# Performance work log

Measured on AMD Instinct MI355X. Metric: run time of the kernel, lower is better.

The kernel has to match this reference:

```python
import jax, jax.numpy as jnp
import numpy as np

EOS = 1e-10
N_NODES = 100000
N_EDGES = 1600000
IN_DIM = 256
HID = 64
ALPHA = 0.1
TEMP = 1.0
BIAS = 1e-4


def setup_inputs() -> dict:
    key = jax.random.key(0)
    k1, k2, k3, k4, k5 = jax.random.split(key, 5)
    features = jax.random.normal(k1, (N_NODES, IN_DIM), dtype=jnp.float32)
    edges = jax.random.randint(k2, (2, N_EDGES), 0, N_NODES, dtype=jnp.int64)
    noise = jax.random.uniform(k3, (N_EDGES,), dtype=jnp.float32)
    # params: embedding Linear(input_dim, hidden) and edge_mlp Linear(2*hidden, 1)
    W_emb = jax.random.normal(k4, (IN_DIM, HID), dtype=jnp.float32) / np.sqrt(IN_DIM)
    b_emb = jnp.zeros((HID,), dtype=jnp.float32)
    W_edge = jax.random.normal(k5, (2 * HID,), dtype=jnp.float32) / np.sqrt(2 * HID)
    b_edge = jnp.zeros((), dtype=jnp.float32)
    return {"features": features, "edges": edges, "noise": noise,
            "W_emb": W_emb, "b_emb": b_emb, "W_edge": W_edge, "b_edge": b_edge}


def _edge_weight_norm_both(src, dst, w, n_nodes):
    # DGL EdgeWeightNorm(norm='both'): w_e / sqrt(outdeg_w(src) * indeg_w(dst))
    deg_out = jax.ops.segment_sum(w, src, num_segments=n_nodes)
    deg_in = jax.ops.segment_sum(w, dst, num_segments=n_nodes)
    return w / jnp.sqrt(deg_out[src] * deg_in[dst])


def reference(features, edges, noise, W_emb, b_emb, W_edge, b_edge):
    src, dst = edges[0], edges[1]
    E = src.shape[0]
    # node embedding: relu(Linear(features))
    h = jax.nn.relu(features @ W_emb + b_emb)  # [N, H]
    # edge score: edge_mlp(cat(h[u], h[v])) symmetrized.
    # split W_edge -> score = h[u]@W1 + h[v]@W2 + b  (avoids materializing concat)
    p1 = h @ W_edge[:HID]   # [N]
    p2 = h @ W_edge[HID:]   # [N]
    s1 = p1[src] + p2[dst] + b_edge
    s2 = p1[dst] + p2[src] + b_edge
    raw = (s1 + s2) * 0.5   # [E]
    # gumbel sigmoid sampling
    eps = (BIAS - (1.0 - BIAS)) * noise + (1.0 - BIAS)
    gate = jnp.log(eps) - jnp.log1p(-eps)
    weights_lp = jax.nn.sigmoid((gate + raw) / TEMP)  # [E]
    weights_hp = 1.0 - weights_lp
    # weight_to_adj: add self loops with weight 1, then EdgeWeightNorm 'both'
    loop = jnp.arange(N_NODES, dtype=src.dtype)
    src_f = jnp.concatenate([src, loop])
    dst_f = jnp.concatenate([dst, loop])
    ones_n = jnp.ones((N_NODES,), dtype=weights_lp.dtype)
    w_lp_full = jnp.concatenate([weights_lp, ones_n]) + EOS
    w_lp_norm = _edge_weight_norm_both(src_f, dst_f, w_lp_full, N_NODES)
    w_hp_full = jnp.concatenate([weights_hp, ones_n]) + EOS
    w_hp_norm = _edge_weight_norm_both(src_f, dst_f, w_hp_full, N_NODES)
    w_hp_norm = w_hp_norm * (-ALPHA)
    w_hp_norm = w_hp_norm.at[E:].set(1.0)  # self-loop weights forced to 1
    return (w_lp_norm, w_hp_norm, weights_lp, weights_hp)
```

## Files before the change

kernel.cpp:

```cpp
#include <hip/hip_runtime.h>
#include <hip/hip_bf16.h>
#include <math.h>

#define N_NODESC 100000
#define N_EDGESC 1600000
#define IN_DIMC 256
#define HIDC 64
#define ALPHAC 0.1f
#define BIASC 1e-4f
#define EOSC 1e-10f

#define MC (N_EDGESC + N_NODESC)
#define NBUCK 25
#define BCAP 68000u
#define W20SCALE 1048576.0f
#define W20INV (1.0f / 1048576.0f)
#define SUMMASK ((1ull << 40) - 1)
#define CNTONE (1ull << 40)

typedef __attribute__((ext_vector_type(8))) short short8;
typedef __attribute__((ext_vector_type(4))) float f32x4;

#define WT_STRIDE 264

__device__ inline void load_edge(const int* __restrict__ edges, int e, int is64,
                                 int& src, int& dst) {
    if (is64) {
        const int2 a = ((const int2*)edges)[e];
        const int2 b = ((const int2*)edges)[N_EDGESC + e];
        src = a.x; dst = b.x;
    } else {
        src = edges[e];
        dst = edges[N_EDGESC + e];
    }
}

__device__ inline short pkbf(float x) {
    union { __hip_bfloat16 b; short s; } u;
    u.b = __float2bfloat16(x);
    return u.s;
}

__global__ __launch_bounds__(256, 4) void node_kernel(
    const float* __restrict__ features,
    const float* __restrict__ W_emb,
    const float* __restrict__ b_emb,
    const float* __restrict__ W_edge,
    const int* __restrict__ edges,
    float* __restrict__ q,
    int* __restrict__ flag) {
    __shared__ __align__(16) short Wt[HIDC * WT_STRIDE];
    const int tid = threadIdx.x;
    if (blockIdx.x == 0 && tid == 0) {
        int z = 0;
        #pragma unroll
        for (int i = 0; i < 16; ++i) z |= edges[2 * i + 1];
        *flag = (z == 0) ? 1 : 0;
    }
    {
        const float4* Wg = (const float4*)W_emb;
        #pragma unroll
        for (int i = 0; i < 16; ++i) {
            const int f4 = tid + 256 * i;
            const float4 g = Wg[f4];
            const int flat = 4 * f4;
            const int k = flat >> 6;
            const int j0 = flat & 63;
            Wt[(j0 + 0) * WT_STRIDE + k] = pkbf(g.x);
            Wt[(j0 + 1) * WT_STRIDE + k] = pkbf(g.y);
            Wt[(j0 + 2) * WT_STRIDE + k] = pkbf(g.z);
            Wt[(j0 + 3) * WT_STRIDE + k] = pkbf(g.w);
        }
    }
    const int lane = tid & 63;
    const int wave = tid >> 6;
    const int quad = lane >> 4;
    const int m = lane & 15;
    f32x4 acc[4];
    float wsum4[4];
    #pragma unroll
    for (int nt = 0; nt < 4; ++nt) {
        const int j = m + 16 * nt;
        const float b = b_emb[j];
        acc[nt] = (f32x4){b, b, b, b};
        wsum4[nt] = W_edge[j] + W_edge[HIDC + j];
    }
    __syncthreads();

    const int node0 = blockIdx.x * 64 + wave * 16;
    const int row = min(node0 + m, N_NODESC - 1);
    const float* frow = features + (size_t)row * IN_DIMC;

    #pragma unroll
    for (int ks = 0; ks < 8; ++ks) {
        const int kk = ks * 32 + quad * 8;
        const float4 fa = *(const float4*)(frow + kk);
        const float4 fb = *(const float4*)(frow + kk + 4);
        short8 af;
        af[0] = pkbf(fa.x); af[1] = pkbf(fa.y);
        af[2] = pkbf(fa.z); af[3] = pkbf(fa.w);
        af[4] = pkbf(fb.x); af[5] = pkbf(fb.y);
        af[6] = pkbf(fb.z); af[7] = pkbf(fb.w);
        #pragma unroll
        for (int nt = 0; nt < 4; ++nt) {
            const short8 bf =
                *(const short8*)&Wt[(m + 16 * nt) * WT_STRIDE + kk];
            acc[nt] = __builtin_amdgcn_mfma_f32_16x16x32_bf16(af, bf, acc[nt],
                                                              0, 0, 0);
        }
    }

    #pragma unroll
    for (int r = 0; r < 4; ++r) {
        float s = 0.f;
        #pragma unroll
        for (int nt = 0; nt < 4; ++nt)
            s = fmaf(fmaxf(acc[nt][r], 0.f), wsum4[nt], s);
        s += __shfl_xor(s, 1);
        s += __shfl_xor(s, 2);
        s += __shfl_xor(s, 4);
        s += __shfl_xor(s, 8);
        if (m == 0) {
            const int node = node0 + quad * 4 + r;
            if (node < N_NODESC) q[node] = s;
        }
    }
}

__global__ __launch_bounds__(256) void edge_scatter(
    const int* __restrict__ edges,
    const float* __restrict__ noise,
    const float* __restrict__ b_edge,
    const float* __restrict__ q,
    unsigned* __restrict__ cursorS,
    unsigned* __restrict__ cursorD,
    float* __restrict__ out,
    const int* __restrict__ flag) {
    __shared__ unsigned histS[NBUCK], histD[NBUCK];
    __shared__ unsigned baseS[NBUCK], baseD[NBUCK];
    const int tid = threadIdx.x;
    if (tid < NBUCK) { histS[tid] = 0; histD[tid] = 0; }
    __syncthreads();
    const int is64 = *flag;
    const float be = b_edge[0];
    int srcA[4], dstA[4];
    float wlpA[4];
    unsigned rkS[4], rkD[4];
    const int e0 = blockIdx.x * 1024 + tid;
    #pragma unroll
    for (int i = 0; i < 4; ++i) {
        const int e = e0 + i * 256;
        srcA[i] = -1;
        if (e < N_EDGESC) {
            int s, d;
            load_edge(edges, e, is64, s, d);
            srcA[i] = s; dstA[i] = d;
            const float raw = 0.5f * (q[s] + q[d]) + be;
            const float u = noise[e];
            const float eps = (BIASC - (1.0f - BIASC)) * u + (1.0f - BIASC);
            const float gate = logf(eps) - log1pf(-eps);
            const float wlp = 1.0f / (1.0f + expf(-(gate + raw)));
            wlpA[i] = wlp;
            out[2 * MC + e] = wlp;
            out[2 * MC + N_EDGESC + e] = 1.0f - wlp;
            rkS[i] = atomicAdd(&histS[s >> 12], 1u);
            rkD[i] = atomicAdd(&histD[d >> 12], 1u);
        }
    }
    __syncthreads();
    if (tid < NBUCK)
        baseS[tid] = atomicAdd(&cursorS[tid], histS[tid]);
    else if (tid < 2 * NBUCK)
        baseD[tid - NBUCK] = atomicAdd(&cursorD[tid - NBUCK], histD[tid - NBUCK]);
    __syncthreads();
    unsigned* recS = (unsigned*)out;
    unsigned* recD = (unsigned*)out + MC;
    #pragma unroll
    for (int i = 0; i < 4; ++i) {
        if (srcA[i] >= 0) {
            const int s = srcA[i], d = dstA[i];
            const unsigned w20 =
                min((unsigned)(wlpA[i] * W20SCALE + 0.5f), 0xFFFFFu);
            const unsigned pS = baseS[s >> 12] + rkS[i];
            const unsigned pD = baseD[d >> 12] + rkD[i];
            if (pS < BCAP)
                recS[(unsigned)(s >> 12) * BCAP + pS] =
                    ((unsigned)(s & 4095) << 20) | w20;
            if (pD < BCAP)
                recD[(unsigned)(d >> 12) * BCAP + pD] =
                    ((unsigned)(d & 4095) << 20) | w20;
        }
    }
}

__global__ __launch_bounds__(1024) void gather_kernel(
    const float* __restrict__ out,
    const unsigned* __restrict__ cursorS,
    const unsigned* __restrict__ cursorD,
    unsigned long long* __restrict__ accS,
    unsigned long long* __restrict__ accD) {
    __shared__ unsigned long long table[4096];
    const int bid = blockIdx.x;
    const int isD = bid >= NBUCK;
    const int bkt = isD ? bid - NBUCK : bid;
    const unsigned* rec = (const unsigned*)out + (isD ? MC : 0) +
                          (unsigned)bkt * BCAP;
    const unsigned cnt = min((isD ? cursorD : cursorS)[bkt], BCAP);
    const int tid = threadIdx.x;
    #pragma unroll
    for (int i = 0; i < 4; ++i) table[tid + 1024 * i] = 0ull;
    __syncthreads();
    for (unsigned i = tid; i < cnt; i += 1024) {
        const unsigned r = rec[i];
        atomicAdd(&table[r >> 20], CNTONE | (unsigned long long)(r & 0xFFFFFu));
    }
    __syncthreads();
    unsigned long long* acc = isD ? accD : accS;
    const int node0 = bkt << 12;
    #pragma unroll
    for (int i = 0; i < 4; ++i) {
        const int local = tid + 1024 * i;
        const int node = node0 + local;
        if (node < N_NODESC) acc[node] = table[local];
    }
}

__global__ __launch_bounds__(256) void prep_kernel(
    const unsigned long long* __restrict__ accS,
    const unsigned long long* __restrict__ accD,
    float4* __restrict__ rnode) {
    const int n = blockIdx.x * blockDim.x + threadIdx.x;
    if (n >= N_NODESC) return;
    const unsigned long long a = accS[n];
    const unsigned long long b = accD[n];
    const float sumS = (float)(a & SUMMASK) * W20INV;
    const float cntS = (float)(a >> 40);
    const float sumD = (float)(b & SUMMASK) * W20INV;
    const float cntD = (float)(b >> 40);
    float4 r;
    r.x = rsqrtf(1.0f + sumS);
    r.y = rsqrtf(1.0f + sumD);
    r.z = rsqrtf(1.0f + cntS - sumS);
    r.w = rsqrtf(1.0f + cntD - sumD);
    rnode[n] = r;
}

__global__ __launch_bounds__(256) void final_kernel(
    const int* __restrict__ edges,
    const float4* __restrict__ rnode,
    float* __restrict__ out,
    const int* __restrict__ flag) {
    const int i = blockIdx.x * blockDim.x + threadIdx.x;
    if (i >= MC) return;
    if (i < N_EDGESC) {
        const int is64 = *flag;
        int src, dst;
        load_edge(edges, i, is64, src, dst);
        const float wlp = out[2 * MC + i] + EOSC;
        const float whp = out[2 * MC + N_EDGESC + i] + EOSC;
        const float4 rs = rnode[src];
        const float4 rd = rnode[dst];
        out[i] = wlp * rs.x * rd.y;
        out[MC + i] = -ALPHAC * whp * rs.z * rd.w;
    } else {
        const int n = i - N_EDGESC;
        const float4 r = rnode[n];
        out[i] = (1.0f + EOSC) * r.x * r.y;
        out[MC + i] = 1.0f;
    }
}

extern "C" void kernel_launch(void* const* d_in, const int* in_sizes, int n_in,
                              void* d_out, int out_size, void* d_ws, size_t ws_size,
                              hipStream_t stream) {
    const float* features = (const float*)d_in[0];
    const int* edges      = (const int*)d_in[1];
    const float* noise    = (const float*)d_in[2];
    const float* W_emb    = (const float*)d_in[3];
    const float* b_emb    = (const float*)d_in[4];
    const float* W_edge   = (const float*)d_in[5];
    const float* b_edge   = (const float*)d_in[6];
    float* out = (float*)d_out;
    char* ws = (char*)d_ws;

    float* q = (float*)ws;
    unsigned long long* accS = (unsigned long long*)(ws + 400000);
    unsigned long long* accD = accS + N_NODESC;
    float4* rnode = (float4*)(ws + 2000000);
    int* flag = (int*)(ws + 3600000);
    unsigned* cursorS = (unsigned*)(ws + 3600004);
    unsigned* cursorD = cursorS + NBUCK;

    hipMemsetAsync(cursorS, 0, 2 * NBUCK * sizeof(unsigned), stream);
    node_kernel<<<(N_NODESC + 63) / 64, 256, 0, stream>>>(features, W_emb, b_emb,
                                                          W_edge, edges, q, flag);
    edge_scatter<<<(N_EDGESC + 1023) / 1024, 256, 0, stream>>>(
        edges, noise, b_edge, q, cursorS, cursorD, out, flag);
    gather_kernel<<<2 * NBUCK, 1024, 0, stream>>>(out, cursorS, cursorD, accS, accD);
    prep_kernel<<<(N_NODESC + 255) / 256, 256, 0, stream>>>(accS, accD, rnode);
    final_kernel<<<(MC + 255) / 256, 256, 0, stream>>>(edges, rnode, out, flag);
}
```

Measured before the change: 279.4 us.

## Fuse prep into gather, double node tile, finer buckets, per-wave histograms

The prep kernel is folded into the gather kernel, which now writes rsqrt factors as separate float2 arrays for source and destination. The cursor memset moves into node_kernel, dropping one launch. The node kernel handles 128 nodes per block with two accumulator sets, and the scatter uses 50 smaller buckets of 2048 nodes with per-wave shared histograms to reduce LDS atomic contention. Gather now runs 100 blocks with smaller tables, raising parallelism, though the bucket capacity margin is tighter.

```diff
diff --git a/kernel.cpp b/kernel.cpp
--- a/kernel.cpp
+++ b/kernel.cpp
@@ -11,8 +11,10 @@
 #define EOSC 1e-10f
 
 #define MC (N_EDGESC + N_NODESC)
-#define NBUCK 25
-#define BCAP 68000u
+#define NBUCK 50
+#define BSHIFT 11
+#define BMASK 2047
+#define BCAP 34000u
 #define W20SCALE 1048576.0f
 #define W20INV (1.0f / 1048576.0f)
 #define SUMMASK ((1ull << 40) - 1)
@@ -41,21 +43,25 @@
     return u.s;
 }
 
-__global__ __launch_bounds__(256, 4) void node_kernel(
+__global__ __launch_bounds__(256, 3) void node_kernel(
     const float* __restrict__ features,
     const float* __restrict__ W_emb,
     const float* __restrict__ b_emb,
     const float* __restrict__ W_edge,
     const int* __restrict__ edges,
     float* __restrict__ q,
+    unsigned* __restrict__ cursor,
     int* __restrict__ flag) {
     __shared__ __align__(16) short Wt[HIDC * WT_STRIDE];
     const int tid = threadIdx.x;
-    if (blockIdx.x == 0 && tid == 0) {
-        int z = 0;
-        #pragma unroll
-        for (int i = 0; i < 16; ++i) z |= edges[2 * i + 1];
-        *flag = (z == 0) ? 1 : 0;
+    if (blockIdx.x == 0) {
+        if (tid == 0) {
+            int z = 0;
+            #pragma unroll
+            for (int i = 0; i < 16; ++i) z |= edges[2 * i + 1];
+            *flag = (z == 0) ? 1 : 0;
+        }
+        if (tid < 2 * NBUCK) cursor[tid] = 0u;
     }
     {
         const float4* Wg = (const float4*)W_emb;
@@ -76,53 +82,67 @@
     const int wave = tid >> 6;
     const int quad = lane >> 4;
     const int m = lane & 15;
-    f32x4 acc[4];
+    f32x4 accA[4], accB[4];
     float wsum4[4];
     #pragma unroll
     for (int nt = 0; nt < 4; ++nt) {
         const int j = m + 16 * nt;
         const float b = b_emb[j];
-        acc[nt] = (f32x4){b, b, b, b};
+        accA[nt] = (f32x4){b, b, b, b};
+        accB[nt] = (f32x4){b, b, b, b};
         wsum4[nt] = W_edge[j] + W_edge[HIDC + j];
     }
     __syncthreads();
 
-    const int node0 = blockIdx.x * 64 + wave * 16;
-    const int row = min(node0 + m, N_NODESC - 1);
-    const float* frow = features + (size_t)row * IN_DIMC;
+    const int node0A = blockIdx.x * 128 + wave * 16;
+    const int node0B = node0A + 64;
+    const float* frA = features + (size_t)min(node0A + m, N_NODESC - 1) * IN_DIMC;
+    const float* frB = features + (size_t)min(node0B + m, N_NODESC - 1) * IN_DIMC;
 
     #pragma unroll
     for (int ks = 0; ks < 8; ++ks) {
         const int kk = ks * 32 + quad * 8;
-        const float4 fa = *(const float4*)(frow + kk);
-        const float4 fb = *(const float4*)(frow + kk + 4);
-        short8 af;
-        af[0] = pkbf(fa.x); af[1] = pkbf(fa.y);
-        af[2] = pkbf(fa.z); af[3] = pkbf(fa.w);
-        af[4] = pkbf(fb.x); af[5] = pkbf(fb.y);
-        af[6] = pkbf(fb.z); af[7] = pkbf(fb.w);
+        const float4 fa0 = *(const float4*)(frA + kk);
+        const float4 fb0 = *(const float4*)(frA + kk + 4);
+        const float4 fa1 = *(const float4*)(frB + kk);
+        const float4 fb1 = *(const float4*)(frB + kk + 4);
+        short8 afA, afB;
+        afA[0] = pkbf(fa0.x); afA[1] = pkbf(fa0.y);
+        afA[2] = pkbf(fa0.z); afA[3] = pkbf(fa0.w);
+        afA[4] = pkbf(fb0.x); afA[5] = pkbf(fb0.y);
+        afA[6] = pkbf(fb0.z); afA[7] = pkbf(fb0.w);
+        afB[0] = pkbf(fa1.x); afB[1] = pkbf(fa1.y);
+        afB[2] = pkbf(fa1.z); afB[3] = pkbf(fa1.w);
+        afB[4] = pkbf(fb1.x); afB[5] = pkbf(fb1.y);
+        afB[6] = pkbf(fb1.z); afB[7] = pkbf(fb1.w);
         #pragma unroll
         for (int nt = 0; nt < 4; ++nt) {
             const short8 bf =
                 *(const short8*)&Wt[(m + 16 * nt) * WT_STRIDE + kk];
-            acc[nt] = __builtin_amdgcn_mfma_f32_16x16x32_bf16(af, bf, acc[nt],
-                                                              0, 0, 0);
+            accA[nt] = __builtin_amdgcn_mfma_f32_16x16x32_bf16(afA, bf, accA[nt],
+                                                               0, 0, 0);
+            accB[nt] = __builtin_amdgcn_mfma_f32_16x16x32_bf16(afB, bf, accB[nt],
+                                                               0, 0, 0);
         }
     }
 
     #pragma unroll
     for (int r = 0; r < 4; ++r) {
-        float s = 0.f;
+        float sA = 0.f, sB = 0.f;
         #pragma unroll
-        for (int nt = 0; nt < 4; ++nt)
-            s = fmaf(fmaxf(acc[nt][r], 0.f), wsum4[nt], s);
-        s += __shfl_xor(s, 1);
-        s += __shfl_xor(s, 2);
-        s += __shfl_xor(s, 4);
-        s += __shfl_xor(s, 8);
+        for (int nt = 0; nt < 4; ++nt) {
+            sA = fmaf(fmaxf(accA[nt][r], 0.f), wsum4[nt], sA);
+            sB = fmaf(fmaxf(accB[nt][r], 0.f), wsum4[nt], sB);
+        }
+        sA += __shfl_xor(sA, 1); sA += __shfl_xor(sA, 2);
+        sA += __shfl_xor(sA, 4); sA += __shfl_xor(sA, 8);
+        sB += __shfl_xor(sB, 1); sB += __shfl_xor(sB, 2);
+        sB += __shfl_xor(sB, 4); sB += __shfl_xor(sB, 8);
         if (m == 0) {
-            const int node = node0 + quad * 4 + r;
-            if (node < N_NODESC) q[node] = s;
+            const int nA = node0A + quad * 4 + r;
+            const int nB = node0B + quad * 4 + r;
+            if (nA < N_NODESC) q[nA] = sA;
+            if (nB < N_NODESC) q[nB] = sB;
         }
     }
 }
@@ -132,30 +152,39 @@
     const float* __restrict__ noise,
     const float* __restrict__ b_edge,
     const float* __restrict__ q,
-    unsigned* __restrict__ cursorS,
-    unsigned* __restrict__ cursorD,
+    unsigned* __restrict__ cursor,
     float* __restrict__ out,
     const int* __restrict__ flag) {
-    __shared__ unsigned histS[NBUCK], histD[NBUCK];
-    __shared__ unsigned baseS[NBUCK], baseD[NBUCK];
+    __shared__ unsigned hist[2][4][NBUCK];
+    __shared__ unsigned wbase[2][4][NBUCK];
     const int tid = threadIdx.x;
-    if (tid < NBUCK) { histS[tid] = 0; histD[tid] = 0; }
+    const int wave = tid >> 6;
+    for (int i = tid; i < 2 * 4 * NBUCK; i += 256)
+        ((unsigned*)hist)[i] = 0u;
     __syncthreads();
     const int is64 = *flag;
     const float be = b_edge[0];
-    int srcA[4], dstA[4];
+    const int e0 = blockIdx.x * 1024 + tid;
+
+    int sA[4], dA[4];
+    #pragma unroll
+    for (int i = 0; i < 4; ++i) {
+        const int e = e0 + i * 256;
+        sA[i] = -1;
+        if (e < N_EDGESC) load_edge(edges, e, is64, sA[i], dA[i]);
+    }
+    float qs[4], qd[4];
+    #pragma unroll
+    for (int i = 0; i < 4; ++i) {
+        if (sA[i] >= 0) { qs[i] = q[sA[i]]; qd[i] = q[dA[i]]; }
+    }
     float wlpA[4];
     unsigned rkS[4], rkD[4];
-    const int e0 = blockIdx.x * 1024 + tid;
     #pragma unroll
     for (int i = 0; i < 4; ++i) {
-        const int e = e0 + i * 256;
-        srcA[i] = -1;
-        if (e < N_EDGESC) {
-            int s, d;
-            load_edge(edges, e, is64, s, d);
-            srcA[i] = s; dstA[i] = d;
-            const float raw = 0.5f * (q[s] + q[d]) + be;
+        if (sA[i] >= 0) {
+            const int e = e0 + i * 256;
+            const float raw = 0.5f * (qs[i] + qd[i]) + be;
             const float u = noise[e];
             const float eps = (BIASC - (1.0f - BIASC)) * u + (1.0f - BIASC);
             const float gate = logf(eps) - log1pf(-eps);
@@ -163,91 +192,93 @@
             wlpA[i] = wlp;
             out[2 * MC + e] = wlp;
             out[2 * MC + N_EDGESC + e] = 1.0f - wlp;
-            rkS[i] = atomicAdd(&histS[s >> 12], 1u);
-            rkD[i] = atomicAdd(&histD[d >> 12], 1u);
-        }
-    }
-    __syncthreads();
-    if (tid < NBUCK)
-        baseS[tid] = atomicAdd(&cursorS[tid], histS[tid]);
-    else if (tid < 2 * NBUCK)
-        baseD[tid - NBUCK] = atomicAdd(&cursorD[tid - NBUCK], histD[tid - NBUCK]);
+            rkS[i] = atomicAdd(&hist[0][wave][sA[i] >> BSHIFT], 1u);
+            rkD[i] = atomicAdd(&hist[1][wave][dA[i] >> BSHIFT], 1u);
+        }
+    }
+    __syncthreads();
+    if (tid < NBUCK) {
+        const unsigned h0 = hist[0][0][tid], h1 = hist[0][1][tid];
+        const unsigned h2 = hist[0][2][tid], h3 = hist[0][3][tid];
+        const unsigned base = atomicAdd(&cursor[tid], h0 + h1 + h2 + h3);
+        wbase[0][0][tid] = base;
+        wbase[0][1][tid] = base + h0;
+        wbase[0][2][tid] = base + h0 + h1;
+        wbase[0][3][tid] = base + h0 + h1 + h2;
+    } else if (wave == 1 && (tid & 63) < NBUCK) {
+        const int b = tid & 63;
+        const unsigned h0 = hist[1][0][b], h1 = hist[1][1][b];
+        const unsigned h2 = hist[1][2][b], h3 = hist[1][3][b];
+        const unsigned base = atomicAdd(&cursor[NBUCK + b], h0 + h1 + h2 + h3);
+        wbase[1][0][b] = base;
+        wbase[1][1][b] = base + h0;
+        wbase[1][2][b] = base + h0 + h1;
+        wbase[1][3][b] = base + h0 + h1 + h2;
+    }
     __syncthreads();
     unsigned* recS = (unsigned*)out;
     unsigned* recD = (unsigned*)out + MC;
     #pragma unroll
     for (int i = 0; i < 4; ++i) {
-        if (srcA[i] >= 0) {
-            const int s = srcA[i], d = dstA[i];
+        if (sA[i] >= 0) {
+            const int s = sA[i], d = dA[i];
             const unsigned w20 =
                 min((unsigned)(wlpA[i] * W20SCALE + 0.5f), 0xFFFFFu);
-            const unsigned pS = baseS[s >> 12] + rkS[i];
-            const unsigned pD = baseD[d >> 12] + rkD[i];
+            const unsigned pS = wbase[0][wave][s >> BSHIFT] + rkS[i];
+            const unsigned pD = wbase[1][wave][d >> BSHIFT] + rkD[i];
             if (pS < BCAP)
-                recS[(unsigned)(s >> 12) * BCAP + pS] =
-                    ((unsigned)(s & 4095) << 20) | w20;
+                recS[(unsigned)(s >> BSHIFT) * BCAP + pS] =
+                    ((unsigned)(s & BMASK) << 20) | w20;
             if (pD < BCAP)
-                recD[(unsigned)(d >> 12) * BCAP + pD] =
-                    ((unsigned)(d & 4095) << 20) | w20;
+                recD[(unsigned)(d >> BSHIFT) * BCAP + pD] =
+                    ((unsigned)(d & BMASK) << 20) | w20;
         }
     }
 }
 
 __global__ __launch_bounds__(1024) void gather_kernel(
     const float* __restrict__ out,
-    const unsigned* __restrict__ cursorS,
-    const unsigned* __restrict__ cursorD,
-    unsigned long long* __restrict__ accS,
-    unsigned long long* __restrict__ accD) {
-    __shared__ unsigned long long table[4096];
+    const unsigned* __restrict__ cursor,
+    float2* __restrict__ rS,
+    float2* __restrict__ rD) {
+    __shared__ unsigned long long table[2048];
     const int bid = blockIdx.x;
     const int isD = bid >= NBUCK;
     const int bkt = isD ? bid - NBUCK : bid;
     const unsigned* rec = (const unsigned*)out + (isD ? MC : 0) +
                           (unsigned)bkt * BCAP;
-    const unsigned cnt = min((isD ? cursorD : cursorS)[bkt], BCAP);
+    const unsigned cnt = min(cursor[isD ? NBUCK + bkt : bkt], BCAP);
     const int tid = threadIdx.x;
-    #pragma unroll
-    for (int i = 0; i < 4; ++i) table[tid + 1024 * i] = 0ull;
+    table[tid] = 0ull;
+    table[tid + 1024] = 0ull;
     __syncthreads();
     for (unsigned i = tid; i < cnt; i += 1024) {
         const unsigned r = rec[i];
         atomicAdd(&table[r >> 20], CNTONE | (unsigned long long)(r & 0xFFFFFu));
     }
     __syncthreads();
-    unsigned long long* acc = isD ? accD : accS;
-    const int node0 = bkt << 12;
-    #pragma unroll
-    for (int i = 0; i < 4; ++i) {
-        const int local = tid + 1024 * i;
+    float2* dstp = isD ? rD : rS;
+    const int node0 = bkt << BSHIFT;
+    #pragma unroll
+    for (int j = 0; j < 2; ++j) {
+        const int local = tid + 1024 * j;
         const int node = node0 + local;
-        if (node < N_NODESC) acc[node] = table[local];
-    }
-}
-
-__global__ __launch_bounds__(256) void prep_kernel(
-    const unsigned long long* __restrict__ accS,
-    const unsigned long long* __restrict__ accD,
-    float4* __restrict__ rnode) {
-    const int n = blockIdx.x * blockDim.x + threadIdx.x;
-    if (n >= N_NODESC) return;
-    const unsigned long long a = accS[n];
-    const unsigned long long b = accD[n];
-    const float sumS = (float)(a & SUMMASK) * W20INV;
-    const float cntS = (float)(a >> 40);
-    const float sumD = (float)(b & SUMMASK) * W20INV;
-    const float cntD = (float)(b >> 40);
-    float4 r;
-    r.x = rsqrtf(1.0f + sumS);
-    r.y = rsqrtf(1.0f + sumD);
-    r.z = rsqrtf(1.0f + cntS - sumS);
-    r.w = rsqrtf(1.0f + cntD - sumD);
-    rnode[n] = r;
+        if (node < N_NODESC) {
+            const unsigned long long a = table[local];
+            const float sum = (float)(a & SUMMASK) * W20INV;
+            const float cf = (float)(a >> 40);
+            float2 r;
+            r.x = rsqrtf(1.0f + sum);
+            r.y = rsqrtf(1.0f + cf - sum);
+            dstp[node] = r;
+        }
+    }
 }
 
 __global__ __launch_bounds__(256) void final_kernel(
     const int* __restrict__ edges,
-    const float4* __restrict__ rnode,
+    const float2* __restrict__ rS,
+    const float2* __restrict__ rD,
     float* __restrict__ out,
     const int* __restrict__ flag) {
     const int i = blockIdx.x * blockDim.x + threadIdx.x;
@@ -258,14 +289,15 @@
         load_edge(edges, i, is64, src, dst);
         const float wlp = out[2 * MC + i] + EOSC;
         const float whp = out[2 * MC + N_EDGESC + i] + EOSC;
-        const float4 rs = rnode[src];
-        const float4 rd = rnode[dst];
-        out[i] = wlp * rs.x * rd.y;
-        out[MC + i] = -ALPHAC * whp * rs.z * rd.w;
+        const float2 a = rS[src];
+        const float2 b = rD[dst];
+        out[i] = wlp * a.x * b.x;
+        out[MC + i] = -ALPHAC * whp * a.y * b.y;
     } else {
         const int n = i - N_EDGESC;
-        const float4 r = rnode[n];
-        out[i] = (1.0f + EOSC) * r.x * r.y;
+        const float2 a = rS[n];
+        const float2 b = rD[n];
+        out[i] = (1.0f + EOSC) * a.x * b.x;
         out[MC + i] = 1.0f;
     }
 }
@@ -284,19 +316,15 @@
     char* ws = (char*)d_ws;
 
     float* q = (float*)ws;
-    unsigned long long* accS = (unsigned long long*)(ws + 400000);
-    unsigned long long* accD = accS + N_NODESC;
-    float4* rnode = (float4*)(ws + 2000000);
+    float2* rS = (float2*)(ws + 400000);
+    float2* rD = (float2*)(ws + 1200000);
     int* flag = (int*)(ws + 3600000);
-    unsigned* cursorS = (unsigned*)(ws + 3600004);
-    unsigned* cursorD = cursorS + NBUCK;
-
-    hipMemsetAsync(cursorS, 0, 2 * NBUCK * sizeof(unsigned), stream);
-    node_kernel<<<(N_NODESC + 63) / 64, 256, 0, stream>>>(features, W_emb, b_emb,
-                                                          W_edge, edges, q, flag);
+    unsigned* cursor = (unsigned*)(ws + 3600004);
+
+    node_kernel<<<782, 256, 0, stream>>>(features, W_emb, b_emb, W_edge, edges,
+                                         q, cursor, flag);
     edge_scatter<<<(N_EDGESC + 1023) / 1024, 256, 0, stream>>>(
-        edges, noise, b_edge, q, cursorS, cursorD, out, flag);
-    gather_kernel<<<2 * NBUCK, 1024, 0, stream>>>(out, cursorS, cursorD, accS, accD);
-    prep_kernel<<<(N_NODESC + 255) / 256, 256, 0, stream>>>(accS, accD, rnode);
-    final_kernel<<<(MC + 255) / 256, 256, 0, stream>>>(edges, rnode, out, flag);
-}
+        edges, noise, b_edge, q, cursor, out, flag);
+    gather_kernel<<<2 * NBUCK, 1024, 0, stream>>>(out, cursor, rS, rD);
+    final_kernel<<<(MC + 255) / 256, 256, 0, stream>>>(edges, rS, rD, out, flag);
+}
```

Measured after the change: 271.1 us. 3.0% less time.
